# Kernel tuning notes

Measured on AMD Instinct MI355X. Metric: run time of the kernel, lower is better.

## Reference

```python
import jax, jax.numpy as jnp
import numpy as np

B, T, V, D, DH, H = 4, 512, 32000, 768, 768, 4  # batch, seq, vocab, dim_in, dim_out(per-head & ffn), heads


def layer_norm(x, g, b, eps=1e-5):
    m = jnp.mean(x, axis=-1, keepdims=True)
    v = jnp.mean((x - m) ** 2, axis=-1, keepdims=True)
    return (x - m) * jax.lax.rsqrt(v + eps) * g + b


def setup_inputs() -> dict:
    key = jax.random.key(0)
    ks = jax.random.split(key, 20)
    s = 0.02
    f = lambda k, shp: (jax.random.normal(k, shp, jnp.float32) * s)
    return {
        "x": jax.random.randint(ks[0], (B, T), 0, V),
        "attention_mask": jax.random.randint(ks[1], (B, 1, T), 0, 2).astype(bool),
        "token_embed": f(ks[2], (V, D)),
        "segment_embed": f(ks[3], (V, D)),
        "ln_embed_g": jnp.ones((D,), jnp.float32), "ln_embed_b": jnp.zeros((D,), jnp.float32),
        "Wq": f(ks[4], (H, D, DH)), "bq": f(ks[5], (H, DH)),
        "Wk": f(ks[6], (H, D, DH)), "bk": f(ks[7], (H, DH)),
        "Wv": f(ks[8], (H, D, DH)), "bv": f(ks[9], (H, DH)),
        "Wo": f(ks[10], (H * DH, D)), "bo": f(ks[11], (D,)),
        "ln_attn_g": jnp.ones((D,), jnp.float32), "ln_attn_b": jnp.zeros((D,), jnp.float32),
        "W1": f(ks[12], (D, DH)), "b1": f(ks[13], (DH,)),
        "W2": f(ks[14], (DH, D)), "b2": f(ks[15], (D,)),
        "ln_enc_g": jnp.ones((D,), jnp.float32), "ln_enc_b": jnp.zeros((D,), jnp.float32),
        "Wproj": f(ks[16], (D, V)), "bproj": f(ks[17], (V,)),
        "Wcls": f(ks[18], (D, 2)), "bcls": f(ks[19], (2,)),
    }


def reference(x, attention_mask, token_embed, segment_embed, ln_embed_g, ln_embed_b,
              Wq, bq, Wk, bk, Wv, bv, Wo, bo, ln_attn_g, ln_attn_b,
              W1, b1, W2, b2, ln_enc_g, ln_enc_b, Wproj, bproj, Wcls, bcls):
    Bsz, Tlen = x.shape
    dim = token_embed.shape[1]
    # JointEmbedding: segment tensor is 0 for first half, 1 afterwards
    seg = jnp.zeros_like(x).at[:, Tlen // 2 + 1:].set(1)
    # positional encoding (faithful to source: exponent is 2*j/dim per column j,
    # sin on even columns, cos on odd columns, applied to pos/10000**exp)
    d = 2.0 * jnp.arange(dim, dtype=jnp.float32) / dim            # [D]
    p = jnp.arange(Tlen, dtype=jnp.float32)[:, None] / (10000.0 ** d)  # [T, D]
    pe = jnp.where(jnp.arange(dim) % 2 == 0, jnp.sin(p), jnp.cos(p))   # [T, D]
    emb = token_embed[x] + segment_embed[seg] + pe[None]          # [B, T, D]
    emb = layer_norm(emb, ln_embed_g, ln_embed_b)

    # Multi-head attention (vectorized over the per-head Python loop)
    Q = jnp.einsum('btd,hde->bhte', emb, Wq) + bq[None, :, None, :]
    K = jnp.einsum('btd,hde->bhte', emb, Wk) + bk[None, :, None, :]
    Vh = jnp.einsum('btd,hde->bhte', emb, Wv) + bv[None, :, None, :]
    # NOTE: source scales by seq_len**-0.5 (Q.size(1)), not head_dim**-0.5
    scores = jnp.einsum('bhte,bhse->bhts', Q, K) * (float(Tlen) ** -0.5)
    # NOTE: source masked_fill_'s with value 1e-9 (not -inf) before softmax
    scores = jnp.where(attention_mask[:, None, :, :], 1e-9, scores)
    attn = jax.nn.softmax(scores, axis=-1)
    ctx = jnp.einsum('bhts,bhse->bhte', attn, Vh)                 # [B, H, T, DH]
    cat = ctx.transpose(0, 2, 1, 3).reshape(Bsz, Tlen, -1)        # head concat order
    attn_out = layer_norm(cat @ Wo + bo, ln_attn_g, ln_attn_b)

    # FFN (no residual in source; dropout is identity at inference)
    h = jax.nn.gelu(attn_out @ W1 + b1, approximate=False)
    enc = layer_norm(h @ W2 + b2, ln_enc_g, ln_enc_b)

    token_pred = enc @ Wproj + bproj                              # [B, T, V]
    logits = jax.nn.log_softmax(token_pred, axis=-1)
    cls_out = enc[:, 0, :] @ Wcls + bcls                          # [B, 2]
    return logits, cls_out
```

## Files before the change

kernel.cpp:

```cpp
#include <hip/hip_runtime.h>
#include <hip/hip_bf16.h>
#include <stdint.h>

#define B_ 4
#define T_ 512
#define V_ 32000
#define D_ 768
#define DH_ 768
#define H_ 4
#define R_ 2048

typedef unsigned short u16;
typedef __attribute__((ext_vector_type(4))) float f32x4;
typedef __attribute__((ext_vector_type(8))) short s16x8;
typedef __attribute__((ext_vector_type(8))) unsigned short u16x8;
typedef __attribute__((address_space(3))) char* lds_cp;
typedef const __attribute__((address_space(1))) char* gl_cp;

__device__ __forceinline__ float bf2f(u16 u){
  union { float f; unsigned int i; } w; w.i = ((unsigned int)u) << 16; return w.f;
}
__device__ __forceinline__ u16 f2bf(float f){
  union { float f; unsigned int i; } w; w.f = f;
  unsigned int r = w.i + 0x7fffu + ((w.i >> 16) & 1u);
  return (u16)(r >> 16);
}

__device__ __forceinline__ float block_sum(float v, float* red){
  #pragma unroll
  for (int o = 32; o; o >>= 1) v += __shfl_down(v, o);
  __syncthreads();
  if ((threadIdx.x & 63) == 0) red[threadIdx.x >> 6] = v;
  __syncthreads();
  return red[0] + red[1] + red[2] + red[3];
}
__device__ __forceinline__ float block_max(float v, float* red){
  #pragma unroll
  for (int o = 32; o; o >>= 1) v = fmaxf(v, __shfl_down(v, o));
  __syncthreads();
  if ((threadIdx.x & 63) == 0) red[threadIdx.x >> 6] = v;
  __syncthreads();
  return fmaxf(fmaxf(red[0], red[1]), fmaxf(red[2], red[3]));
}

__global__ void mask_convert(const void* __restrict__ mraw, int* __restrict__ mout){
  __shared__ int isbyte;
  if (threadIdx.x == 0) isbyte = 0;
  __syncthreads();
  const unsigned char* by = (const unsigned char*)mraw;
  int f = 0;
  for (int i = threadIdx.x; i < 2048; i += 256)
    if ((i & 3) && by[i]) f = 1;
  if (f) atomicOr(&isbyte, 1);
  __syncthreads();
  if (isbyte){
    for (int i = threadIdx.x; i < 2048; i += 256) mout[i] = by[i] ? 1 : 0;
  } else {
    const int* mi = (const int*)mraw;
    for (int i = threadIdx.x; i < 2048; i += 256) mout[i] = mi[i] ? 1 : 0;
  }
}

__global__ __launch_bounds__(256)
void transpose_all(const float* __restrict__ Wq, const float* __restrict__ Wk,
                   const float* __restrict__ Wv, const float* __restrict__ Wo,
                   const float* __restrict__ W1, const float* __restrict__ W2,
                   u16* __restrict__ wqT, u16* __restrict__ wkT,
                   u16* __restrict__ wvT, u16* __restrict__ woT,
                   u16* __restrict__ w1T, u16* __restrict__ w2T){
  __shared__ u16 tile[32][33];
  int z = blockIdx.z;
  const float* in; u16* out; int out_ld = 768;
  if (z < 4)      { in = Wq + (long)z * 589824;        out = wqT + (long)z * 589824; }
  else if (z < 8) { int k = z - 4;  in = Wk + (long)k * 589824; out = wkT + (long)k * 589824; }
  else if (z < 12){ int k = z - 8;  in = Wv + (long)k * 589824; out = wvT + (long)k * 589824; }
  else if (z < 16){ int k = z - 12; in = Wo + (long)k * 589824; out = woT + (long)k * 768; out_ld = 3072; }
  else if (z == 16){ in = W1; out = w1T; }
  else             { in = W2; out = w2T; }
  int c0 = blockIdx.x * 32, r0 = blockIdx.y * 32;
  int tx = threadIdx.x & 31, ty = threadIdx.x >> 5;
  #pragma unroll
  for (int i = 0; i < 32; i += 8)
    tile[ty + i][tx] = f2bf(in[(long)(r0 + ty + i) * 768 + (c0 + tx)]);
  __syncthreads();
  #pragma unroll
  for (int i = 0; i < 32; i += 8)
    out[(long)(c0 + ty + i) * out_ld + (r0 + tx)] = tile[tx][ty + i];
}

__global__ __launch_bounds__(256)
void transpose_f2b(const float* __restrict__ in, u16* __restrict__ out, int R, int C){
  __shared__ u16 tile[32][33];
  int c0 = blockIdx.x * 32, r0 = blockIdx.y * 32;
  int tx = threadIdx.x & 31, ty = threadIdx.x >> 5;
  #pragma unroll
  for (int i = 0; i < 32; i += 8)
    tile[ty + i][tx] = f2bf(in[(long)(r0 + ty + i) * C + (c0 + tx)]);
  __syncthreads();
  #pragma unroll
  for (int i = 0; i < 32; i += 8)
    out[(long)(c0 + ty + i) * R + (r0 + tx)] = tile[tx][ty + i];
}

__global__ __launch_bounds__(256)
void embed_ln(const int* __restrict__ x, const float* __restrict__ tok,
              const float* __restrict__ seg, const float* __restrict__ g,
              const float* __restrict__ bb, u16* __restrict__ emb){
  __shared__ float red[4];
  int r = blockIdx.x, t = r & 511;
  int tid = threadIdx.x;
  long trow = (long)x[r] * D_;
  long srow = (t > 256) ? (long)D_ : 0;
  float v[3];
  float s = 0.f;
  #pragma unroll
  for (int q = 0; q < 3; ++q){
    int j = tid + q * 256;
    float d = (2.0f * (float)j) * (1.0f / 768.0f);
    float p = (float)t * powf(10000.0f, -d);
    float pe = (j & 1) ? cosf(p) : sinf(p);
    v[q] = tok[trow + j] + seg[srow + j] + pe;
    s += v[q];
  }
  float mean = block_sum(s, red) * (1.0f / 768.0f);
  float vs = 0.f;
  #pragma unroll
  for (int q = 0; q < 3; ++q){ float dd = v[q] - mean; vs += dd * dd; }
  float var = block_sum(vs, red) * (1.0f / 768.0f);
  float inv = rsqrtf(var + 1e-5f);
  #pragma unroll
  for (int q = 0; q < 3; ++q){
    int j = tid + q * 256;
    emb[(long)r * D_ + j] = f2bf((v[q] - mean) * inv * g[j] + bb[j]);
  }
}

__global__ __launch_bounds__(256)
void ln_rows(const u16* __restrict__ in, const float* __restrict__ g,
             const float* __restrict__ bb, u16* __restrict__ out){
  __shared__ float red[4];
  long r = blockIdx.x;
  int tid = threadIdx.x;
  const u16* row = in + r * D_;
  float v[3];
  float s = 0.f;
  #pragma unroll
  for (int q = 0; q < 3; ++q){ v[q] = bf2f(row[tid + q * 256]); s += v[q]; }
  float mean = block_sum(s, red) * (1.0f / 768.0f);
  float vs = 0.f;
  #pragma unroll
  for (int q = 0; q < 3; ++q){ float dd = v[q] - mean; vs += dd * dd; }
  float var = block_sum(vs, red) * (1.0f / 768.0f);
  float inv = rsqrtf(var + 1e-5f);
  #pragma unroll
  for (int q = 0; q < 3; ++q){
    int j = tid + q * 256;
    out[r * D_ + j] = f2bf((v[q] - mean) * inv * g[j] + bb[j]);
  }
}

__global__ __launch_bounds__(256)
void attn_softmax(u16* __restrict__ S, const int* __restrict__ mask){
  __shared__ float red[4];
  int t = blockIdx.x, z = blockIdx.y, b = z >> 2;
  u16* row = S + (long)z * (T_ * T_) + (long)t * T_;
  int tid = threadIdx.x;
  int s0 = tid, s1 = tid + 256;
  float v0 = mask[b * T_ + s0] ? 1e-9f : bf2f(row[s0]);
  float v1 = mask[b * T_ + s1] ? 1e-9f : bf2f(row[s1]);
  float mx = block_max(fmaxf(v0, v1), red);
  float e0 = expf(v0 - mx), e1 = expf(v1 - mx);
  float l = block_sum(e0 + e1, red);
  float inv = 1.0f / l;
  row[s0] = f2bf(e0 * inv);
  row[s1] = f2bf(e1 * inv);
}

__global__ __launch_bounds__(256)
void lsm_b2f(const u16* __restrict__ pred, float* __restrict__ out){
  __shared__ float sm[256], sl[256];
  long r = blockIdx.x;
  const u16x8* rv = (const u16x8*)(pred + r * (long)V_);
  int tid = threadIdx.x;
  float m = -1e30f, l = 0.f;
  for (int c = tid; c < V_ / 8; c += 256){
    u16x8 v = rv[c];
    #pragma unroll
    for (int j = 0; j < 8; ++j){
      float x = bf2f(v[j]);
      if (x > m){ l = l * expf(m - x) + 1.0f; m = x; }
      else l += expf(x - m);
    }
  }
  sm[tid] = m; sl[tid] = l;
  __syncthreads();
  #pragma unroll
  for (int s = 128; s; s >>= 1){
    if (tid < s){
      float m2 = sm[tid + s], l2 = sl[tid + s];
      float M = fmaxf(sm[tid], m2);
      sl[tid] = sl[tid] * expf(sm[tid] - M) + l2 * expf(m2 - M);
      sm[tid] = M;
    }
    __syncthreads();
  }
  float lse = sm[0] + logf(sl[0]);
  f32x4* orow = (f32x4*)(out + r * (long)V_);
  for (int c = tid; c < V_ / 8; c += 256){
    u16x8 v = rv[c];
    f32x4 o0, o1;
    #pragma unroll
    for (int j = 0; j < 4; ++j){ o0[j] = bf2f(v[j]) - lse; o1[j] = bf2f(v[j + 4]) - lse; }
    orow[2 * c] = o0; orow[2 * c + 1] = o1;
  }
}

__global__ __launch_bounds__(256)
void log_softmax_rows(float* __restrict__ tp){
  __shared__ float sm[256], sl[256];
  long r = blockIdx.x;
  float* row = tp + r * (long)V_;
  f32x4* rv = (f32x4*)row;
  int tid = threadIdx.x;
  float m = -1e30f, l = 0.f;
  for (int c = tid; c < V_ / 4; c += 256){
    f32x4 v = rv[c];
    #pragma unroll
    for (int j = 0; j < 4; ++j){
      float x = v[j];
      if (x > m){ l = l * expf(m - x) + 1.0f; m = x; }
      else l += expf(x - m);
    }
  }
  sm[tid] = m; sl[tid] = l;
  __syncthreads();
  #pragma unroll
  for (int s = 128; s; s >>= 1){
    if (tid < s){
      float m2 = sm[tid + s], l2 = sl[tid + s];
      float M = fmaxf(sm[tid], m2);
      sl[tid] = sl[tid] * expf(sm[tid] - M) + l2 * expf(m2 - M);
      sm[tid] = M;
    }
    __syncthreads();
  }
  float lse = sm[0] + logf(sl[0]);
  for (int c = tid; c < V_ / 4; c += 256){
    f32x4 v = rv[c];
    #pragma unroll
    for (int j = 0; j < 4; ++j) v[j] -= lse;
    rv[c] = v;
  }
}

__global__ __launch_bounds__(256)
void cls_head(const u16* __restrict__ enc, const float* __restrict__ Wc,
              const float* __restrict__ bc, float* __restrict__ out){
  int w = threadIdx.x >> 6, lane = threadIdx.x & 63;
  const u16* e = enc + (long)w * (T_ * D_);
  float a0 = 0.f, a1 = 0.f;
  for (int k = lane; k < D_; k += 64){
    float ev = bf2f(e[k]);
    a0 += ev * Wc[k * 2 + 0];
    a1 += ev * Wc[k * 2 + 1];
  }
  #pragma unroll
  for (int o = 32; o; o >>= 1){ a0 += __shfl_down(a0, o); a1 += __shfl_down(a1, o); }
  if (lane == 0){
    out[(long)B_ * T_ * V_ + w * 2 + 0] = a0 + bc[0];
    out[(long)B_ * T_ * V_ + w * 2 + 1] = a1 + bc[1];
  }
}

template<int GELU, int F32OUT>
__global__ __launch_bounds__(256, 2)
void gemm_bt(const u16* __restrict__ A, const u16* __restrict__ Bt,
             const float* __restrict__ bias, void* __restrict__ Cv,
             int lda, int ldb,
             long sAzb, long sAzh, long sBzb, long sBzh, long sbz,
             long sCzb, long sCzh, long sCb, long sCr, long sCc,
             int zsh, float scale, int nt){
  extern __shared__ char smem[];
  u16* sA = (u16*)smem;
  u16* sB = sA + 2 * 128 * 64;
  int tid = threadIdx.x, lane = tid & 63, wid = tid >> 6;
  int wm = wid >> 1, wn = wid & 1;
  int lrow = lane & 15, lquad = lane >> 4;

  unsigned gx = gridDim.x, gy = gridDim.y;
  unsigned nwg = gx * gy * gridDim.z;
  unsigned id = blockIdx.x + gx * (blockIdx.y + gy * blockIdx.z);
  unsigned qq = nwg >> 3, rr = nwg & 7, xcd = id & 7, loc = id >> 3;
  unsigned nid = (xcd < rr ? xcd * (qq + 1) : rr * (qq + 1) + (xcd - rr) * qq) + loc;
  unsigned bx = nid % gx, tmpq = nid / gx;
  unsigned by = tmpq % gy, bz = tmpq / gy;

  int z = (int)bz, zb = z >> zsh, zh = z & ((1 << zsh) - 1);
  long bm = (long)bx * 128, bn = (long)by * 128;
  const u16* Az = A + zb * sAzb + zh * sAzh;
  const u16* Bz = Bt + zb * sBzb + zh * sBzh;

  f32x4 acc[4][4] = {};

  auto stage = [&](int buf, int kt){
    #pragma unroll
    for (int q = 0; q < 4; ++q){
      int seg = wid * 4 + q;
      int idx = seg * 64 + lane;
      int r = idx >> 3, c = idx & 7;
      int ksw = (c ^ (r & 7)) << 3;
      const u16* srcA = Az + (bm + r) * lda + kt * 64 + ksw;
      const u16* srcB = Bz + (bn + r) * ldb + kt * 64 + ksw;
      __builtin_amdgcn_global_load_lds((gl_cp)srcA,
          (lds_cp)((char*)(sA + buf * 8192) + seg * 1024), 16, 0, 0);
      __builtin_amdgcn_global_load_lds((gl_cp)srcB,
          (lds_cp)((char*)(sB + buf * 8192) + seg * 1024), 16, 0, 0);
    }
  };

  stage(0, 0);
  __syncthreads();
  int cur = 0;
  for (int t = 0; t < nt; ++t){
    if (t + 1 < nt) stage(cur ^ 1, t + 1);
    const u16* a0 = sA + cur * 8192;
    const u16* b0 = sB + cur * 8192;
    #pragma unroll
    for (int kk = 0; kk < 2; ++kk){
      int koff = (((kk * 4 + lquad) ^ (lrow & 7)) << 3);
      s16x8 af[4], bfv[4];
      #pragma unroll
      for (int m = 0; m < 4; ++m)
        af[m] = *(const s16x8*)(a0 + (wm * 64 + m * 16 + lrow) * 64 + koff);
      #pragma unroll
      for (int n = 0; n < 4; ++n)
        bfv[n] = *(const s16x8*)(b0 + (wn * 64 + n * 16 + lrow) * 64 + koff);
      #pragma unroll
      for (int m = 0; m < 4; ++m)
        #pragma unroll
        for (int n = 0; n < 4; ++n)
          acc[m][n] = __builtin_amdgcn_mfma_f32_16x16x32_bf16(af[m], bfv[n], acc[m][n], 0, 0, 0);
    }
    __syncthreads();
    cur ^= 1;
  }

  long czbase = zb * sCzb + zh * sCzh;
  #pragma unroll
  for (int n = 0; n < 4; ++n){
    long col = bn + wn * 64 + n * 16 + lrow;
    float bv = bias ? bias[zb * sbz + col] : 0.f;
    #pragma unroll
    for (int m = 0; m < 4; ++m){
      #pragma unroll
      for (int j = 0; j < 4; ++j){
        long row = bm + wm * 64 + m * 16 + lquad * 4 + j;
        float v = acc[m][n][j] * scale + bv;
        if (GELU) v = 0.5f * v * (1.0f + erff(v * 0.70710678118654752f));
        long ci = czbase + (row >> 9) * sCb + (row & 511) * sCr + col * sCc;
        if (F32OUT) ((float*)Cv)[ci] = v;
        else        ((u16*)Cv)[ci] = f2bf(v);
      }
    }
  }
}

extern "C" void kernel_launch(void* const* d_in, const int* in_sizes, int n_in,
                              void* d_out, int out_size, void* d_ws, size_t ws_size,
                              hipStream_t stream){
  const int*   x     = (const int*)d_in[0];
  const void*  amask = d_in[1];
  const float* tok = (const float*)d_in[2];
  const float* seg = (const float*)d_in[3];
  const float* lng = (const float*)d_in[4];
  const float* lnb = (const float*)d_in[5];
  const float* Wq  = (const float*)d_in[6];
  const float* bq  = (const float*)d_in[7];
  const float* Wk  = (const float*)d_in[8];
  const float* bk  = (const float*)d_in[9];
  const float* Wv  = (const float*)d_in[10];
  const float* bv  = (const float*)d_in[11];
  const float* Wo  = (const float*)d_in[12];
  const float* bo  = (const float*)d_in[13];
  const float* lag = (const float*)d_in[14];
  const float* lab = (const float*)d_in[15];
  const float* W1  = (const float*)d_in[16];
  const float* b1  = (const float*)d_in[17];
  const float* W2  = (const float*)d_in[18];
  const float* b2  = (const float*)d_in[19];
  const float* leg = (const float*)d_in[20];
  const float* leb = (const float*)d_in[21];
  const float* Wp  = (const float*)d_in[22];
  const float* bp  = (const float*)d_in[23];
  const float* Wc  = (const float*)d_in[24];
  const float* bc  = (const float*)d_in[25];
  float* out = (float*)d_out;
  char* ws = (char*)d_ws;

  size_t off = 0;
  auto alloc = [&](size_t bytes){ size_t o = off; off += (bytes + 255) & ~(size_t)255; return o; };
  size_t o_mask = alloc(2048 * 4);
  size_t o_emb  = alloc((size_t)R_ * D_ * 2);
  size_t o_wqT  = alloc((size_t)H_ * D_ * DH_ * 2);
  size_t o_wkT  = alloc((size_t)H_ * D_ * DH_ * 2);
  size_t o_wvT  = alloc((size_t)H_ * D_ * DH_ * 2);
  size_t o_woT  = alloc((size_t)3072 * 768 * 2);
  size_t o_w1T  = alloc((size_t)768 * 768 * 2);
  size_t o_w2T  = alloc((size_t)768 * 768 * 2);
  size_t o_Q    = alloc((size_t)B_ * H_ * T_ * DH_ * 2);
  size_t o_K    = alloc((size_t)B_ * H_ * T_ * DH_ * 2);
  size_t o_VT   = alloc((size_t)B_ * H_ * DH_ * T_ * 2);
  size_t o_S    = alloc((size_t)B_ * H_ * T_ * T_ * 2);
  size_t o_cat  = alloc((size_t)R_ * 3072 * 2);
  size_t o_ap   = alloc((size_t)R_ * D_ * 2);
  size_t o_ao   = alloc((size_t)R_ * D_ * 2);
  size_t o_h1   = alloc((size_t)R_ * D_ * 2);
  size_t o_ep   = alloc((size_t)R_ * D_ * 2);
  size_t o_enc  = alloc((size_t)R_ * D_ * 2);
  size_t o_wpT  = o_Q;
  size_t off_base = off;
  size_t o_pred = alloc((size_t)R_ * V_ * 2);
  int bigws = (ws_size >= off);
  if (ws_size < off_base) return;

  int* maskI = (int*)(ws + o_mask);
  u16* emb  = (u16*)(ws + o_emb);
  u16* wqT  = (u16*)(ws + o_wqT);
  u16* wkT  = (u16*)(ws + o_wkT);
  u16* wvT  = (u16*)(ws + o_wvT);
  u16* woT  = (u16*)(ws + o_woT);
  u16* w1T  = (u16*)(ws + o_w1T);
  u16* w2T  = (u16*)(ws + o_w2T);
  u16* Qb   = (u16*)(ws + o_Q);
  u16* Kb   = (u16*)(ws + o_K);
  u16* VTb  = (u16*)(ws + o_VT);
  u16* Sb   = (u16*)(ws + o_S);
  u16* catb = (u16*)(ws + o_cat);
  u16* apb  = (u16*)(ws + o_ap);
  u16* aob  = (u16*)(ws + o_ao);
  u16* h1b  = (u16*)(ws + o_h1);
  u16* epb  = (u16*)(ws + o_ep);
  u16* encb = (u16*)(ws + o_enc);
  u16* wpT  = (u16*)(ws + o_wpT);
  u16* predb = (u16*)(ws + o_pred);

  const long sQK_zb = (long)H_ * T_ * DH_;
  const long sQK_zh = (long)T_ * DH_;

  mask_convert<<<1, 256, 0, stream>>>(amask, maskI);
  transpose_all<<<dim3(24, 24, 18), 256, 0, stream>>>(Wq, Wk, Wv, Wo, W1, W2,
      wqT, wkT, wvT, woT, w1T, w2T);
  embed_ln<<<R_, 256, 0, stream>>>(x, tok, seg, lng, lnb, emb);

  gemm_bt<0,0><<<dim3(16, 6, 4), 256, 65536, stream>>>(emb, wqT, bq, Qb,
      768, 768, 0, 0, (long)768 * 768, 0, 768,
      sQK_zh, 0, sQK_zb, 768, 1, 0, 1.0f, 12);
  gemm_bt<0,0><<<dim3(16, 6, 4), 256, 65536, stream>>>(emb, wkT, bk, Kb,
      768, 768, 0, 0, (long)768 * 768, 0, 768,
      sQK_zh, 0, sQK_zb, 768, 1, 0, 1.0f, 12);
  gemm_bt<0,0><<<dim3(16, 6, 4), 256, 65536, stream>>>(emb, wvT, bv, VTb,
      768, 768, 0, 0, (long)768 * 768, 0, 768,
      sQK_zh, 0, sQK_zb, 1, 512, 0, 1.0f, 12);

  gemm_bt<0,0><<<dim3(4, 4, 16), 256, 65536, stream>>>(Qb, Kb, nullptr, Sb,
      768, 768, sQK_zb, sQK_zh, sQK_zb, sQK_zh, 0,
      (long)H_ * T_ * T_, (long)T_ * T_, 0, 512, 1, 2, 0.044194173824159216f, 12);

  attn_softmax<<<dim3(512, 16), 256, 0, stream>>>(Sb, maskI);

  gemm_bt<0,0><<<dim3(4, 6, 16), 256, 65536, stream>>>(Sb, VTb, nullptr, catb,
      512, 512, (long)H_ * T_ * T_, (long)T_ * T_, sQK_zb, sQK_zh, 0,
      (long)T_ * 3072, 768, 0, 3072, 1, 2, 1.0f, 8);

  gemm_bt<0,0><<<dim3(16, 6, 1), 256, 65536, stream>>>(catb, woT, bo, apb,
      3072, 3072, 0, 0, 0, 0, 0,
      0, 0, (long)512 * 768, 768, 1, 0, 1.0f, 48);
  ln_rows<<<R_, 256, 0, stream>>>(apb, lag, lab, aob);

  gemm_bt<1,0><<<dim3(16, 6, 1), 256, 65536, stream>>>(aob, w1T, b1, h1b,
      768, 768, 0, 0, 0, 0, 0,
      0, 0, (long)512 * 768, 768, 1, 0, 1.0f, 12);
  gemm_bt<0,0><<<dim3(16, 6, 1), 256, 65536, stream>>>(h1b, w2T, b2, epb,
      768, 768, 0, 0, 0, 0, 0,
      0, 0, (long)512 * 768, 768, 1, 0, 1.0f, 12);
  ln_rows<<<R_, 256, 0, stream>>>(epb, leg, leb, encb);

  transpose_f2b<<<dim3(1000, 24, 1), 256, 0, stream>>>(Wp, wpT, 768, 32000);

  if (bigws){
    gemm_bt<0,0><<<dim3(16, 250, 1), 256, 65536, stream>>>(encb, wpT, bp, predb,
        768, 768, 0, 0, 0, 0, 0,
        0, 0, (long)512 * V_, V_, 1, 0, 1.0f, 12);
    lsm_b2f<<<R_, 256, 0, stream>>>(predb, out);
  } else {
    gemm_bt<0,1><<<dim3(16, 250, 1), 256, 65536, stream>>>(encb, wpT, bp, out,
        768, 768, 0, 0, 0, 0, 0,
        0, 0, (long)512 * V_, V_, 1, 0, 1.0f, 12);
    log_softmax_rows<<<R_, 256, 0, stream>>>(out);
  }
  cls_head<<<1, 256, 0, stream>>>(encb, Wc, bc, out);

  (void)in_sizes; (void)n_in; (void)out_size;
}
```

Baseline: 486.0 us.

## Add 256x256-tile 8-wave GEMM with 4-slot LDS pipeline for vocab projection

Replaces the generic 128x128 GEMM used for the 2048x32000x768 vocabulary projection with a dedicated kernel. It uses 256x256 tiles, 8 waves, and a 4-slot LDS ring fed by direct global-to-LDS loads with three k-steps in flight. Each k-step is split into two MFMA phases that are interleaved with staging, and setprio is raised around the MFMA blocks. The aim is higher arithmetic intensity and better overlap of loads with MFMA work, at the cost of 128KB LDS per block, a large accumulator register footprint, and a grid of 1000 blocks that may leave tail imbalance.

Measured after the change: 507.2 us. +4.3%, slower.

```diff
diff --git a/kernel.cpp b/kernel.cpp
--- a/kernel.cpp
+++ b/kernel.cpp
@@ -360,6 +360,104 @@
         long ci = czbase + (row >> 9) * sCb + (row & 511) * sCr + col * sCc;
         if (F32OUT) ((float*)Cv)[ci] = v;
         else        ((u16*)Cv)[ci] = f2bf(v);
+      }
+    }
+  }
+}
+
+template<int F32OUT>
+__global__ __launch_bounds__(512, 2)
+void gemm8p(const u16* __restrict__ A, const u16* __restrict__ Bt,
+            const float* __restrict__ bias, void* __restrict__ Cv){
+  __shared__ char smem[131072];
+  const int tid = threadIdx.x, lane = tid & 63, wid = tid >> 6;
+  const int wm = wid >> 2, wn = wid & 3;
+  const int lrow = lane & 15, lquad = lane >> 4;
+  const long bm = (long)blockIdx.x * 256, bn = (long)blockIdx.y * 256;
+  const int NT = 24;
+
+  f32x4 acc[8][4] = {};
+
+  auto stage_half = [&](int k, int kind, int h){
+    int slot = k & 3;
+    int r = tid >> 2, c = tid & 3;
+    int lc = c ^ (r & 3);
+    const u16* src = (kind ? Bt + (bn + h * 128 + r) * 768
+                           : A  + (bm + h * 128 + r) * 768) + k * 32 + lc * 8;
+    char* dst = smem + slot * 32768 + kind * 16384 + h * 8192 + (wid * 64) * 16;
+    __builtin_amdgcn_global_load_lds((gl_cp)src, (lds_cp)dst, 16, 0, 0);
+  };
+
+  #pragma unroll
+  for (int k = 0; k < 3; ++k){
+    stage_half(k, 0, 0); stage_half(k, 0, 1);
+    stage_half(k, 1, 0); stage_half(k, 1, 1);
+  }
+  asm volatile("s_waitcnt vmcnt(8)" ::: "memory");
+  __builtin_amdgcn_s_barrier();
+  __builtin_amdgcn_sched_barrier(0);
+
+  const int ksw = (lquad ^ (lrow & 3)) * 16;
+  for (int k = 0; k < NT; ++k){
+    const char* slot = smem + (k & 3) * 32768;
+    const char* aBase = slot + wm * 8192;
+    const char* bBase = slot + 16384 + (wn >> 1) * 8192 + ((wn & 1) * 64) * 64;
+    s16x8 af[4], bfv[4];
+
+    #pragma unroll
+    for (int nf = 0; nf < 4; ++nf)
+      bfv[nf] = *(const s16x8*)(bBase + (nf * 16 + lrow) * 64 + ksw);
+    #pragma unroll
+    for (int mf = 0; mf < 4; ++mf)
+      af[mf] = *(const s16x8*)(aBase + (mf * 16 + lrow) * 64 + ksw);
+    if (k + 3 < NT){ stage_half(k + 3, 0, 0); stage_half(k + 3, 0, 1); }
+    __builtin_amdgcn_s_barrier();
+    asm volatile("s_waitcnt lgkmcnt(0)" ::: "memory");
+    __builtin_amdgcn_sched_barrier(0);
+    __builtin_amdgcn_s_setprio(1);
+    #pragma unroll
+    for (int mf = 0; mf < 4; ++mf)
+      #pragma unroll
+      for (int nf = 0; nf < 4; ++nf)
+        acc[mf][nf] = __builtin_amdgcn_mfma_f32_16x16x32_bf16(af[mf], bfv[nf], acc[mf][nf], 0, 0, 0);
+    __builtin_amdgcn_s_setprio(0);
+    __builtin_amdgcn_sched_barrier(0);
+    __builtin_amdgcn_s_barrier();
+
+    #pragma unroll
+    for (int mf = 0; mf < 4; ++mf)
+      af[mf] = *(const s16x8*)(aBase + ((mf + 4) * 16 + lrow) * 64 + ksw);
+    if (k + 3 < NT){ stage_half(k + 3, 1, 0); stage_half(k + 3, 1, 1); }
+    __builtin_amdgcn_s_barrier();
+    asm volatile("s_waitcnt lgkmcnt(0)" ::: "memory");
+    __builtin_amdgcn_sched_barrier(0);
+    __builtin_amdgcn_s_setprio(1);
+    #pragma unroll
+    for (int mf = 0; mf < 4; ++mf)
+      #pragma unroll
+      for (int nf = 0; nf < 4; ++nf)
+        acc[mf + 4][nf] = __builtin_amdgcn_mfma_f32_16x16x32_bf16(af[mf], bfv[nf], acc[mf + 4][nf], 0, 0, 0);
+    __builtin_amdgcn_s_setprio(0);
+    __builtin_amdgcn_sched_barrier(0);
+    if (k <= NT - 4)      { asm volatile("s_waitcnt vmcnt(8)" ::: "memory"); }
+    else if (k == NT - 3) { asm volatile("s_waitcnt vmcnt(4)" ::: "memory"); }
+    else if (k == NT - 2) { asm volatile("s_waitcnt vmcnt(0)" ::: "memory"); }
+    __builtin_amdgcn_s_barrier();
+    __builtin_amdgcn_sched_barrier(0);
+  }
+
+  #pragma unroll
+  for (int nf = 0; nf < 4; ++nf){
+    long col = bn + wn * 64 + nf * 16 + lrow;
+    float bv = bias[col];
+    #pragma unroll
+    for (int mf = 0; mf < 8; ++mf){
+      #pragma unroll
+      for (int j = 0; j < 4; ++j){
+        long row = bm + wm * 128 + mf * 16 + lquad * 4 + j;
+        float v = acc[mf][nf][j] + bv;
+        if (F32OUT) ((float*)Cv)[row * (long)V_ + col] = v;
+        else        ((u16*)Cv)[row * (long)V_ + col] = f2bf(v);
       }
     }
   }
@@ -488,14 +586,10 @@
   transpose_f2b<<<dim3(1000, 24, 1), 256, 0, stream>>>(Wp, wpT, 768, 32000);
 
   if (bigws){
-    gemm_bt<0,0><<<dim3(16, 250, 1), 256, 65536, stream>>>(encb, wpT, bp, predb,
-        768, 768, 0, 0, 0, 0, 0,
-        0, 0, (long)512 * V_, V_, 1, 0, 1.0f, 12);
+    gemm8p<0><<<dim3(8, 125), 512, 0, stream>>>(encb, wpT, bp, predb);
     lsm_b2f<<<R_, 256, 0, stream>>>(predb, out);
   } else {
-    gemm_bt<0,1><<<dim3(16, 250, 1), 256, 65536, stream>>>(encb, wpT, bp, out,
-        768, 768, 0, 0, 0, 0, 0,
-        0, 0, (long)512 * V_, V_, 1, 0, 1.0f, 12);
+    gemm8p<1><<<dim3(8, 125), 512, 0, stream>>>(encb, wpT, bp, out);
     log_softmax_rows<<<R_, 256, 0, stream>>>(out);
   }
   cls_head<<<1, 256, 0, stream>>>(encb, Wc, bc, out);
```

## Add specialized vocab-projection GEMM with smaller LDS, XCD-aware block remap

Applied to the files above, without the earlier changes.

Replaces the generic batched gemm_bt for the 2048x32000x768 vocab projection with a dedicated kernel. It uses 32 KB of static LDS with K-tile 32 instead of 64 KB dynamic, and launch bounds of 4 blocks per CU to raise occupancy. It also remaps block ids so consecutive workgroups on the same XCD share B/A tiles in cache, and hardcodes strides to cut index arithmetic. The risk is more K iterations with more barriers, and less work per sync.

Result: slower. 502.8 us (+3.5%).

```diff
diff --git a/kernel.cpp b/kernel.cpp
--- a/kernel.cpp
+++ b/kernel.cpp
@@ -360,6 +360,79 @@
         long ci = czbase + (row >> 9) * sCb + (row & 511) * sCr + col * sCc;
         if (F32OUT) ((float*)Cv)[ci] = v;
         else        ((u16*)Cv)[ci] = f2bf(v);
+      }
+    }
+  }
+}
+
+template<int F32OUT>
+__global__ __launch_bounds__(256, 4)
+void gemm_wp(const u16* __restrict__ A, const u16* __restrict__ Bt,
+             const float* __restrict__ bias, void* __restrict__ Cv){
+  __shared__ char smem[32768];
+  const int tid = threadIdx.x, lane = tid & 63, wid = tid >> 6;
+  const int wm = wid >> 1, wn = wid & 1;
+  const int lrow = lane & 15, lquad = lane >> 4;
+
+  unsigned id = blockIdx.x + 16u * blockIdx.y;
+  unsigned wg = (id & 7u) * 500u + (id >> 3);
+  const long bm = (long)(wg & 15u) * 128;
+  const long bn = (long)(wg >> 4) * 128;
+  const int NT = 24;
+
+  f32x4 acc[4][4] = {};
+
+  auto stage = [&](int slot, int kt){
+    #pragma unroll
+    for (int q = 0; q < 2; ++q){
+      int idx = q * 256 + tid;
+      int r = idx >> 2, c = idx & 3;
+      int lc = c ^ ((r >> 1) & 3);
+      const u16* srcA = A + (bm + r) * 768 + kt * 32 + lc * 8;
+      const u16* srcB = Bt + (bn + r) * 768 + kt * 32 + lc * 8;
+      __builtin_amdgcn_global_load_lds((gl_cp)srcA,
+          (lds_cp)(smem + slot * 16384 + idx * 16), 16, 0, 0);
+      __builtin_amdgcn_global_load_lds((gl_cp)srcB,
+          (lds_cp)(smem + slot * 16384 + 8192 + idx * 16), 16, 0, 0);
+    }
+  };
+
+  stage(0, 0);
+  __syncthreads();
+  const int koff = (lquad ^ ((lrow >> 1) & 3)) * 16;
+  int cur = 0;
+  for (int t = 0; t < NT; ++t){
+    if (t + 1 < NT) stage(cur ^ 1, t + 1);
+    const char* a0 = smem + cur * 16384;
+    const char* b0 = a0 + 8192;
+    s16x8 af[4], bfv[4];
+    #pragma unroll
+    for (int m = 0; m < 4; ++m)
+      af[m] = *(const s16x8*)(a0 + (wm * 64 + m * 16 + lrow) * 64 + koff);
+    #pragma unroll
+    for (int n = 0; n < 4; ++n)
+      bfv[n] = *(const s16x8*)(b0 + (wn * 64 + n * 16 + lrow) * 64 + koff);
+    #pragma unroll
+    for (int m = 0; m < 4; ++m)
+      #pragma unroll
+      for (int n = 0; n < 4; ++n)
+        acc[m][n] = __builtin_amdgcn_mfma_f32_16x16x32_bf16(af[m], bfv[n], acc[m][n], 0, 0, 0);
+    __syncthreads();
+    cur ^= 1;
+  }
+
+  #pragma unroll
+  for (int n = 0; n < 4; ++n){
+    long col = bn + wn * 64 + n * 16 + lrow;
+    float bv = bias[col];
+    #pragma unroll
+    for (int m = 0; m < 4; ++m){
+      #pragma unroll
+      for (int j = 0; j < 4; ++j){
+        long row = bm + wm * 64 + m * 16 + lquad * 4 + j;
+        float v = acc[m][n][j] + bv;
+        if (F32OUT) ((float*)Cv)[row * (long)V_ + col] = v;
+        else        ((u16*)Cv)[row * (long)V_ + col] = f2bf(v);
       }
     }
   }
@@ -488,14 +561,10 @@
   transpose_f2b<<<dim3(1000, 24, 1), 256, 0, stream>>>(Wp, wpT, 768, 32000);
 
   if (bigws){
-    gemm_bt<0,0><<<dim3(16, 250, 1), 256, 65536, stream>>>(encb, wpT, bp, predb,
-        768, 768, 0, 0, 0, 0, 0,
-        0, 0, (long)512 * V_, V_, 1, 0, 1.0f, 12);
+    gemm_wp<0><<<dim3(16, 250), 256, 0, stream>>>(encb, wpT, bp, predb);
     lsm_b2f<<<R_, 256, 0, stream>>>(predb, out);
   } else {
-    gemm_bt<0,1><<<dim3(16, 250, 1), 256, 65536, stream>>>(encb, wpT, bp, out,
-        768, 768, 0, 0, 0, 0, 0,
-        0, 0, (long)512 * V_, V_, 1, 0, 1.0f, 12);
+    gemm_wp<1><<<dim3(16, 250), 256, 0, stream>>>(encb, wpT, bp, out);
     log_softmax_rows<<<R_, 256, 0, stream>>>(out);
   }
   cls_head<<<1, 256, 0, stream>>>(encb, Wc, bc, out);
```
